# Kernel optimization log

Hardware: AMD Instinct MI355X
Metric: run time of the kernel (lower is better)

## Reference

```python
import jax, jax.numpy as jnp
import numpy as np

WORLD_SIZE = 8
BS = 16
MSG = 16384


def setup_inputs() -> dict:
    key = jax.random.key(0)
    k0, k1, kw, kb = jax.random.split(key, 4)
    x0 = jax.random.normal(k0, (WORLD_SIZE, BS, MSG), dtype=jnp.float32)
    x1 = jax.random.normal(k1, (WORLD_SIZE, BS, MSG), dtype=jnp.float32)
    # nn.Linear(msg_size, msg_size) params, kaiming-uniform-ish scale
    scale = 1.0 / np.sqrt(MSG)
    W = jax.random.uniform(kw, (MSG, MSG), dtype=jnp.float32, minval=-scale, maxval=scale)
    b = jax.random.uniform(kb, (MSG,), dtype=jnp.float32, minval=-scale, maxval=scale)
    return {"x0": x0, "x1": x1, "W": W, "b": b}


def reference(x0, x1, W, b):
    # all_gather_ll: concat per-rank shards along dim 0 -> [world_size*bs, msg]
    t0 = x0.reshape(WORLD_SIZE * BS, MSG)
    t1 = x1.reshape(WORLD_SIZE * BS, MSG)
    # shared Linear applied to both gathered tensors: y = t @ W^T + b
    y0 = jnp.einsum("nk,mk->nm", t0, W) + b
    y1 = jnp.einsum("nk,mk->nm", t1, W) + b
    return (y0, y1)
```

## Files before the change

### kernel.cpp

```cpp
#include <hip/hip_runtime.h>
#include <hip/hip_bf16.h>

typedef __bf16 bf16x8 __attribute__((ext_vector_type(8)));
typedef float  f32x4  __attribute__((ext_vector_type(4)));

#define N_TOT   16384
#define K_TOT   16384
#define HALF_M  ((size_t)128 * 16384)
#define BN      128
#define BK      64
#define KSPLIT  4
#define KQ_LEN  (K_TOT / KSPLIT)
#define NQSTEPS (KQ_LEN / BK)
#define OUT_ELEMS ((size_t)256 * 16384)

__device__ __forceinline__ unsigned short f2bf(float f) {
    __hip_bfloat16 h = __float2bfloat16(f);
    return __builtin_bit_cast(unsigned short, h);
}

__device__ __forceinline__ int swz(int row, int g) {
    return row * 128 + (((g ^ (row & 7)) & 7) << 4);
}

__global__ void cvtT_kernel(const float* __restrict__ x0,
                            const float* __restrict__ x1,
                            unsigned short* __restrict__ wsT) {
    size_t i = (size_t)blockIdx.x * blockDim.x + threadIdx.x;
    size_t e = i * 8;
    const float* src = (e < HALF_M) ? (x0 + e) : (x1 + (e - HALF_M));
    float4 a = ((const float4*)src)[0];
    float4 b = ((const float4*)src)[1];
    union { unsigned short u[8]; uint4 v; } o;
    o.u[0] = f2bf(a.x); o.u[1] = f2bf(a.y); o.u[2] = f2bf(a.z); o.u[3] = f2bf(a.w);
    o.u[4] = f2bf(b.x); o.u[5] = f2bf(b.y); o.u[6] = f2bf(b.z); o.u[7] = f2bf(b.w);
    ((uint4*)wsT)[i] = o.v;
}

__global__ void combine_kernel(float* __restrict__ out,
                               const float* __restrict__ p0,
                               const float* __restrict__ p1,
                               const float* __restrict__ p2) {
    const size_t n4 = OUT_ELEMS / 4;
    size_t i = (size_t)blockIdx.x * blockDim.x + threadIdx.x;
    for (; i < n4; i += (size_t)gridDim.x * blockDim.x) {
        float4 o = ((const float4*)out)[i];
        float4 a = ((const float4*)p0)[i];
        float4 b = ((const float4*)p1)[i];
        float4 c = ((const float4*)p2)[i];
        o.x += a.x + b.x + c.x;  o.y += a.y + b.y + c.y;
        o.z += a.z + b.z + c.z;  o.w += a.w + b.w + c.w;
        ((float4*)out)[i] = o;
    }
}

#define ISSUEW(S, k0) do {                                                    \
    const uint4* _p = (const uint4*)(arow_w + (k0));                          \
    w##S##_0 = _p[0]; w##S##_1 = _p[1];                                       \
    const float4* _q = (const float4*)(brow + (k0));                          \
    wb##S##_0 = _q[0]; wb##S##_1 = _q[1];                                     \
} while (0)

#define STAGEW(S, Ab, Bb) do {                                                \
    *(uint4*)((Ab) + aw0) = w##S##_0;                                         \
    *(uint4*)((Ab) + aw1) = w##S##_1;                                         \
    union { unsigned short u[8]; uint4 v; } _tb;                              \
    _tb.u[0]=f2bf(wb##S##_0.x); _tb.u[1]=f2bf(wb##S##_0.y);                   \
    _tb.u[2]=f2bf(wb##S##_0.z); _tb.u[3]=f2bf(wb##S##_0.w);                   \
    _tb.u[4]=f2bf(wb##S##_1.x); _tb.u[5]=f2bf(wb##S##_1.y);                   \
    _tb.u[6]=f2bf(wb##S##_1.z); _tb.u[7]=f2bf(wb##S##_1.w);                   \
    *(uint4*)((Bb) + bw) = _tb.v;                                             \
} while (0)

#define COMPUTE(Ab, Bb) do {                                                  \
    bf16x8 _b00 = *(const bf16x8*)((Bb) + boff00);                            \
    bf16x8 _b01 = *(const bf16x8*)((Bb) + boff01);                            \
    bf16x8 _b10 = *(const bf16x8*)((Bb) + boff10);                            \
    bf16x8 _b11 = *(const bf16x8*)((Bb) + boff11);                            \
    bf16x8 _a;                                                                \
    _a = *(const bf16x8*)((Ab) + aoff00);                                     \
    acc00 = __builtin_amdgcn_mfma_f32_16x16x32_bf16(_a, _b00, acc00, 0, 0, 0);\
    acc01 = __builtin_amdgcn_mfma_f32_16x16x32_bf16(_a, _b10, acc01, 0, 0, 0);\
    _a = *(const bf16x8*)((Ab) + aoff01);                                     \
    acc00 = __builtin_amdgcn_mfma_f32_16x16x32_bf16(_a, _b01, acc00, 0, 0, 0);\
    acc01 = __builtin_amdgcn_mfma_f32_16x16x32_bf16(_a, _b11, acc01, 0, 0, 0);\
    _a = *(const bf16x8*)((Ab) + aoff10);                                     \
    acc10 = __builtin_amdgcn_mfma_f32_16x16x32_bf16(_a, _b00, acc10, 0, 0, 0);\
    acc11 = __builtin_amdgcn_mfma_f32_16x16x32_bf16(_a, _b10, acc11, 0, 0, 0);\
    _a = *(const bf16x8*)((Ab) + aoff11);                                     \
    acc10 = __builtin_amdgcn_mfma_f32_16x16x32_bf16(_a, _b01, acc10, 0, 0, 0);\
    acc11 = __builtin_amdgcn_mfma_f32_16x16x32_bf16(_a, _b11, acc11, 0, 0, 0);\
    _a = *(const bf16x8*)((Ab) + aoff20);                                     \
    acc20 = __builtin_amdgcn_mfma_f32_16x16x32_bf16(_a, _b00, acc20, 0, 0, 0);\
    acc21 = __builtin_amdgcn_mfma_f32_16x16x32_bf16(_a, _b10, acc21, 0, 0, 0);\
    _a = *(const bf16x8*)((Ab) + aoff21);                                     \
    acc20 = __builtin_amdgcn_mfma_f32_16x16x32_bf16(_a, _b01, acc20, 0, 0, 0);\
    acc21 = __builtin_amdgcn_mfma_f32_16x16x32_bf16(_a, _b11, acc21, 0, 0, 0);\
    _a = *(const bf16x8*)((Ab) + aoff30);                                     \
    acc30 = __builtin_amdgcn_mfma_f32_16x16x32_bf16(_a, _b00, acc30, 0, 0, 0);\
    acc31 = __builtin_amdgcn_mfma_f32_16x16x32_bf16(_a, _b10, acc31, 0, 0, 0);\
    _a = *(const bf16x8*)((Ab) + aoff31);                                     \
    acc30 = __builtin_amdgcn_mfma_f32_16x16x32_bf16(_a, _b01, acc30, 0, 0, 0);\
    acc31 = __builtin_amdgcn_mfma_f32_16x16x32_bf16(_a, _b11, acc31, 0, 0, 0);\
} while (0)

#define SYNC do {                                                             \
    asm volatile("s_waitcnt lgkmcnt(0)" ::: "memory");                        \
    __builtin_amdgcn_s_barrier();                                             \
    __builtin_amdgcn_sched_barrier(0);                                        \
} while (0)

__global__ __launch_bounds__(1024, 4)
void gemm_ws(const float* __restrict__ W, const float* __restrict__ bias,
             const unsigned short* __restrict__ wsT,
             float* __restrict__ out, float* __restrict__ wsP)
{
    __shared__ uint4 smem_[(2 * 32768 + 2 * 16384) / 16];
    char* const sm = (char*)smem_;
    char* const A0 = sm;
    char* const A1 = sm + 32768;
    char* const B0 = sm + 65536;
    char* const B1 = sm + 65536 + 16384;

    const int tid  = threadIdx.x;
    const int lane = tid & 63;
    const int wave = tid >> 6;
    const int wm = wave >> 2;
    const int wn = wave & 3;
    const int nstrip = blockIdx.x & 127;
    const int kq     = blockIdx.x >> 7;
    const int n0     = nstrip * BN;
    const int kbase  = kq * KQ_LEN;

    const int ra  = tid >> 2;
    const int pa  = tid & 3;
    const int rbs = tid >> 3;
    const int cbs = (tid & 7) * 8;

    const unsigned short* arow_w = wsT + (size_t)ra * K_TOT + kbase + pa * 16;
    const float* brow = W + (size_t)(n0 + rbs) * K_TOT + kbase + cbs;

    const int aw0 = swz(ra, 2 * pa);
    const int aw1 = swz(ra, 2 * pa + 1);
    const int bw  = swz(rbs, tid & 7);

    const int aoff00 = swz(wm * 64 +  0 + (lane & 15), 0 + (lane >> 4));
    const int aoff01 = swz(wm * 64 +  0 + (lane & 15), 4 + (lane >> 4));
    const int aoff10 = swz(wm * 64 + 16 + (lane & 15), 0 + (lane >> 4));
    const int aoff11 = swz(wm * 64 + 16 + (lane & 15), 4 + (lane >> 4));
    const int aoff20 = swz(wm * 64 + 32 + (lane & 15), 0 + (lane >> 4));
    const int aoff21 = swz(wm * 64 + 32 + (lane & 15), 4 + (lane >> 4));
    const int aoff30 = swz(wm * 64 + 48 + (lane & 15), 0 + (lane >> 4));
    const int aoff31 = swz(wm * 64 + 48 + (lane & 15), 4 + (lane >> 4));
    const int boff00 = swz(wn * 32 +  0 + (lane & 15), 0 + (lane >> 4));
    const int boff01 = swz(wn * 32 +  0 + (lane & 15), 4 + (lane >> 4));
    const int boff10 = swz(wn * 32 + 16 + (lane & 15), 0 + (lane >> 4));
    const int boff11 = swz(wn * 32 + 16 + (lane & 15), 4 + (lane >> 4));

    f32x4 acc00 = {0.f,0.f,0.f,0.f}, acc01 = {0.f,0.f,0.f,0.f};
    f32x4 acc10 = {0.f,0.f,0.f,0.f}, acc11 = {0.f,0.f,0.f,0.f};
    f32x4 acc20 = {0.f,0.f,0.f,0.f}, acc21 = {0.f,0.f,0.f,0.f};
    f32x4 acc30 = {0.f,0.f,0.f,0.f}, acc31 = {0.f,0.f,0.f,0.f};

    uint4  w0_0, w0_1, w1_0, w1_1;
    float4 wb0_0, wb0_1, wb1_0, wb1_1;

    ISSUEW(0, 0);
    ISSUEW(1, BK);
    STAGEW(0, A0, B0);
    SYNC;

    for (int kt = 0; kt < NQSTEPS; kt += 2) {
        if (kt + 2 < NQSTEPS) ISSUEW(0, (kt + 2) * BK);
        COMPUTE(A0, B0);
        STAGEW(1, A1, B1);
        SYNC;
        if (kt + 3 < NQSTEPS) ISSUEW(1, (kt + 3) * BK);
        COMPUTE(A1, B1);
        if (kt + 2 < NQSTEPS) STAGEW(0, A0, B0);
        SYNC;
    }

    float* const dst = (kq == 0) ? out : (wsP + (size_t)(kq - 1) * OUT_ELEMS);
    #pragma unroll
    for (int nf = 0; nf < 2; ++nf) {
        const int col = n0 + wn * 32 + nf * 16 + (lane & 15);
        const float bv = (kq == 0) ? bias[col] : 0.f;
        #pragma unroll
        for (int mf = 0; mf < 4; ++mf) {
            const f32x4 a =
                (nf == 0) ? (mf == 0 ? acc00 : mf == 1 ? acc10 : mf == 2 ? acc20 : acc30)
                          : (mf == 0 ? acc01 : mf == 1 ? acc11 : mf == 2 ? acc21 : acc31);
            #pragma unroll
            for (int j = 0; j < 4; ++j) {
                int r = wm * 64 + mf * 16 + (lane >> 4) * 4 + j;
                float v = a[j] + bv;
                float* o = (r < 128) ? (dst + (size_t)r * N_TOT + col)
                                     : (dst + HALF_M + (size_t)(r - 128) * N_TOT + col);
                *o = v;
            }
        }
    }
}

extern "C" void kernel_launch(void* const* d_in, const int* in_sizes, int n_in,
                              void* d_out, int out_size, void* d_ws, size_t ws_size,
                              hipStream_t stream) {
    const float* x0 = (const float*)d_in[0];
    const float* x1 = (const float*)d_in[1];
    const float* W  = (const float*)d_in[2];
    const float* b  = (const float*)d_in[3];
    float* out = (float*)d_out;

    const size_t wsT_bytes = (size_t)256 * 16384 * sizeof(unsigned short);
    const size_t wsP_bytes = 3 * OUT_ELEMS * sizeof(float);

    unsigned short* wsT = (unsigned short*)d_ws;
    float* wsP = (float*)((char*)d_ws + wsT_bytes);

    (void)wsP_bytes; (void)ws_size;

    cvtT_kernel<<<2048, 256, 0, stream>>>(x0, x1, wsT);
    gemm_ws<<<512, 1024, 0, stream>>>(W, b, wsT, out, wsP);
    combine_kernel<<<2048, 256, 0, stream>>>(out, wsP, wsP + OUT_ELEMS,
                                             wsP + 2 * OUT_ELEMS);
}
```

Before: 282.5 us.

## Pre-tile activations in swizzled layout and DMA them directly into LDS

The conversion kernel now writes bf16 activations as contiguous, pre-swizzled 32 KB k-step tiles. The GEMM loads these tiles with global_load_lds, bypassing registers and the LDS store path, and waits on vmcnt before each barrier. Block-to-(k-quarter, n-strip) mapping is remapped so neighbouring blocks share N strips across k quarters, and the occupancy hint in launch bounds is dropped. This removes register staging for A at the cost of tighter vmcnt ordering and redundant clamped loads in the final iterations.

```diff
diff --git a/kernel.cpp b/kernel.cpp
--- a/kernel.cpp
+++ b/kernel.cpp
@@ -12,6 +12,8 @@
 #define KSPLIT  4
 #define KQ_LEN  (K_TOT / KSPLIT)
 #define NQSTEPS (KQ_LEN / BK)
+#define KSTEPS_TOT (K_TOT / BK)
+#define TILE_BYTES 32768
 #define OUT_ELEMS ((size_t)256 * 16384)
 
 __device__ __forceinline__ unsigned short f2bf(float f) {
@@ -21,14 +23,27 @@
 
 __device__ __forceinline__ int swz(int row, int g) {
     return row * 128 + (((g ^ (row & 7)) & 7) << 4);
+}
+
+__device__ __forceinline__ void load_lds16(const void* g, void* l) {
+    __builtin_amdgcn_global_load_lds(
+        (const __attribute__((address_space(1))) unsigned int*)g,
+        (__attribute__((address_space(3))) unsigned int*)l, 16, 0, 0);
 }
 
 __global__ void cvtT_kernel(const float* __restrict__ x0,
                             const float* __restrict__ x1,
                             unsigned short* __restrict__ wsT) {
     size_t i = (size_t)blockIdx.x * blockDim.x + threadIdx.x;
-    size_t e = i * 8;
-    const float* src = (e < HALF_M) ? (x0 + e) : (x1 + (e - HALF_M));
+    const int ks   = (int)(i >> 11);
+    const int rem  = (int)(i & 2047);
+    const int r    = rem >> 3;
+    const int gimg = rem & 7;
+    const int g    = gimg ^ (r & 7);
+    const float* src = (r < 128)
+        ? (x0 + (size_t)r * K_TOT)
+        : (x1 + (size_t)(r - 128) * K_TOT);
+    src += ks * 64 + g * 8;
     float4 a = ((const float4*)src)[0];
     float4 b = ((const float4*)src)[1];
     union { unsigned short u[8]; uint4 v; } o;
@@ -55,21 +70,23 @@
 }
 
 #define ISSUEW(S, k0) do {                                                    \
-    const uint4* _p = (const uint4*)(arow_w + (k0));                          \
-    w##S##_0 = _p[0]; w##S##_1 = _p[1];                                       \
     const float4* _q = (const float4*)(brow + (k0));                          \
     wb##S##_0 = _q[0]; wb##S##_1 = _q[1];                                     \
 } while (0)
 
-#define STAGEW(S, Ab, Bb) do {                                                \
-    *(uint4*)((Ab) + aw0) = w##S##_0;                                         \
-    *(uint4*)((Ab) + aw1) = w##S##_1;                                         \
+#define STAGEW(S, Bb) do {                                                    \
     union { unsigned short u[8]; uint4 v; } _tb;                              \
     _tb.u[0]=f2bf(wb##S##_0.x); _tb.u[1]=f2bf(wb##S##_0.y);                   \
     _tb.u[2]=f2bf(wb##S##_0.z); _tb.u[3]=f2bf(wb##S##_0.w);                   \
     _tb.u[4]=f2bf(wb##S##_1.x); _tb.u[5]=f2bf(wb##S##_1.y);                   \
     _tb.u[6]=f2bf(wb##S##_1.z); _tb.u[7]=f2bf(wb##S##_1.w);                   \
     *(uint4*)((Bb) + bw) = _tb.v;                                             \
+} while (0)
+
+#define DMA_A(Ab, ks) do {                                                    \
+    const char* _src = (const char*)wsT + (size_t)(ks) * TILE_BYTES + dma_go; \
+    load_lds16(_src,        (Ab) + dma_lo);                                   \
+    load_lds16(_src + 1024, (Ab) + dma_lo + 1024);                            \
 } while (0)
 
 #define COMPUTE(Ab, Bb) do {                                                  \
@@ -104,44 +121,42 @@
     acc31 = __builtin_amdgcn_mfma_f32_16x16x32_bf16(_a, _b11, acc31, 0, 0, 0);\
 } while (0)
 
-#define SYNC do {                                                             \
+#define SYNCC do {                                                            \
+    asm volatile("s_waitcnt vmcnt(2)" ::: "memory");                          \
     asm volatile("s_waitcnt lgkmcnt(0)" ::: "memory");                        \
     __builtin_amdgcn_s_barrier();                                             \
     __builtin_amdgcn_sched_barrier(0);                                        \
 } while (0)
 
-__global__ __launch_bounds__(1024, 4)
+__global__ __launch_bounds__(1024)
 void gemm_ws(const float* __restrict__ W, const float* __restrict__ bias,
              const unsigned short* __restrict__ wsT,
              float* __restrict__ out, float* __restrict__ wsP)
 {
-    __shared__ uint4 smem_[(2 * 32768 + 2 * 16384) / 16];
+    __shared__ uint4 smem_[(2 * TILE_BYTES + 2 * 16384) / 16];
     char* const sm = (char*)smem_;
     char* const A0 = sm;
-    char* const A1 = sm + 32768;
-    char* const B0 = sm + 65536;
-    char* const B1 = sm + 65536 + 16384;
+    char* const A1 = sm + TILE_BYTES;
+    char* const B0 = sm + 2 * TILE_BYTES;
+    char* const B1 = sm + 2 * TILE_BYTES + 16384;
 
     const int tid  = threadIdx.x;
     const int lane = tid & 63;
     const int wave = tid >> 6;
     const int wm = wave >> 2;
     const int wn = wave & 3;
-    const int nstrip = blockIdx.x & 127;
-    const int kq     = blockIdx.x >> 7;
+    const int bid    = blockIdx.x;
+    const int kq     = (bid & 7) >> 1;
+    const int nstrip = ((bid >> 3) << 1) + (bid & 1);
     const int n0     = nstrip * BN;
     const int kbase  = kq * KQ_LEN;
-
-    const int ra  = tid >> 2;
-    const int pa  = tid & 3;
+    const int ks0    = kq * NQSTEPS;
+
+    const int dma_lo = wave * 2048;
+    const int dma_go = wave * 2048 + lane * 16;
+
     const int rbs = tid >> 3;
-    const int cbs = (tid & 7) * 8;
-
-    const unsigned short* arow_w = wsT + (size_t)ra * K_TOT + kbase + pa * 16;
-    const float* brow = W + (size_t)(n0 + rbs) * K_TOT + kbase + cbs;
-
-    const int aw0 = swz(ra, 2 * pa);
-    const int aw1 = swz(ra, 2 * pa + 1);
+    const float* brow = W + (size_t)(n0 + rbs) * K_TOT + kbase + (tid & 7) * 8;
     const int bw  = swz(rbs, tid & 7);
 
     const int aoff00 = swz(wm * 64 +  0 + (lane & 15), 0 + (lane >> 4));
@@ -162,23 +177,36 @@
     f32x4 acc20 = {0.f,0.f,0.f,0.f}, acc21 = {0.f,0.f,0.f,0.f};
     f32x4 acc30 = {0.f,0.f,0.f,0.f}, acc31 = {0.f,0.f,0.f,0.f};
 
-    uint4  w0_0, w0_1, w1_0, w1_1;
     float4 wb0_0, wb0_1, wb1_0, wb1_1;
 
+    DMA_A(A0, ks0);
+    __builtin_amdgcn_sched_barrier(0);
     ISSUEW(0, 0);
     ISSUEW(1, BK);
-    STAGEW(0, A0, B0);
-    SYNC;
+    STAGEW(0, B0);
+    SYNCC;
 
     for (int kt = 0; kt < NQSTEPS; kt += 2) {
-        if (kt + 2 < NQSTEPS) ISSUEW(0, (kt + 2) * BK);
-        COMPUTE(A0, B0);
-        STAGEW(1, A1, B1);
-        SYNC;
-        if (kt + 3 < NQSTEPS) ISSUEW(1, (kt + 3) * BK);
-        COMPUTE(A1, B1);
-        if (kt + 2 < NQSTEPS) STAGEW(0, A0, B0);
-        SYNC;
+        {
+            const int kn = (kt + 1 < NQSTEPS) ? (kt + 1) : (NQSTEPS - 1);
+            DMA_A(A1, ks0 + kn);
+            __builtin_amdgcn_sched_barrier(0);
+            const int kw = ((kt + 2 < NQSTEPS) ? (kt + 2) : (NQSTEPS - 1)) * BK;
+            ISSUEW(0, kw);
+            COMPUTE(A0, B0);
+            STAGEW(1, B1);
+            SYNCC;
+        }
+        {
+            const int kn = (kt + 2 < NQSTEPS) ? (kt + 2) : (NQSTEPS - 1);
+            DMA_A(A0, ks0 + kn);
+            __builtin_amdgcn_sched_barrier(0);
+            const int kw = ((kt + 3 < NQSTEPS) ? (kt + 3) : (NQSTEPS - 1)) * BK;
+            ISSUEW(1, kw);
+            COMPUTE(A1, B1);
+            STAGEW(0, B0);
+            SYNCC;
+        }
     }
 
     float* const dst = (kq == 0) ? out : (wsP + (size_t)(kq - 1) * OUT_ELEMS);
@@ -212,13 +240,10 @@
     const float* b  = (const float*)d_in[3];
     float* out = (float*)d_out;
 
-    const size_t wsT_bytes = (size_t)256 * 16384 * sizeof(unsigned short);
-    const size_t wsP_bytes = 3 * OUT_ELEMS * sizeof(float);
+    const size_t wsT_bytes = (size_t)KSTEPS_TOT * TILE_BYTES;
 
     unsigned short* wsT = (unsigned short*)d_ws;
     float* wsP = (float*)((char*)d_ws + wsT_bytes);
-
-    (void)wsP_bytes; (void)ws_size;
 
     cvtT_kernel<<<2048, 256, 0, stream>>>(x0, x1, wsT);
     gemm_ws<<<512, 1024, 0, stream>>>(W, b, wsT, out, wsP);
```

Measured after the change: 380.7 us. 34.8% more time.
